# Kernel tuning notes

Hardware: AMD Instinct MI355X
Metric: run time of the kernel (lower is better)

The kernel has to match this reference:

```python
import jax, jax.numpy as jnp
import numpy as np

_FP8_MAX = 448.0  # finfo(float8_e4m3fn).max


def _quantize_fp8(w):
    """Per-tensor FP8 quantization: returns fp8-snapped weight (as f32) and scale."""
    scale = jnp.maximum(jnp.max(jnp.abs(w)).astype(jnp.float32) / _FP8_MAX, 1e-12)
    w_q = (w / scale).astype(jnp.float8_e4m3fn).astype(jnp.float32)
    return w_q, scale


def setup_inputs() -> dict:
    key = jax.random.key(0)
    k_x, k_g, k_u, k_d = jax.random.split(key, 4)
    B, S, H, I = 4, 2048, 4096, 11008
    x = jax.random.normal(k_x, (B, S, H), dtype=jnp.float32)
    gate = jax.random.normal(k_g, (I, H), dtype=jnp.float32) * 0.05
    up = jax.random.normal(k_u, (I, H), dtype=jnp.float32) * 0.05
    down = jax.random.normal(k_d, (H, I), dtype=jnp.float32) * 0.05
    gate_w, gate_w_scale = _quantize_fp8(gate)
    up_w, up_w_scale = _quantize_fp8(up)
    down_w, down_w_scale = _quantize_fp8(down)
    one = jnp.float32(1.0)
    return {
        "x": x,
        "gate_w": gate_w, "up_w": up_w, "down_w": down_w,
        "gate_w_scale": gate_w_scale, "up_w_scale": up_w_scale, "down_w_scale": down_w_scale,
        "gate_in_scale": one, "up_in_scale": one, "down_in_scale": one,
    }


def _fake_quant_fp8_linear(x, w_q, in_scale, w_scale):
    # Fake-quantize activations to FP8 (per-tensor scale), dequantize weight, GEMM.
    x_q = jnp.clip(x / in_scale, -_FP8_MAX, _FP8_MAX)
    x_dq = x_q.astype(jnp.float8_e4m3fn).astype(jnp.float32) * in_scale
    w_dq = w_q * w_scale  # w_q values are already on the FP8 grid
    return jnp.einsum('bsh,ih->bsi', x_dq, w_dq)


def reference(x, gate_w, up_w, down_w, gate_w_scale, up_w_scale, down_w_scale,
              gate_in_scale, up_in_scale, down_in_scale):
    gate_out = _fake_quant_fp8_linear(x, gate_w, gate_in_scale, gate_w_scale)
    up_out = _fake_quant_fp8_linear(x, up_w, up_in_scale, up_w_scale)
    hidden = jax.nn.silu(gate_out) * up_out  # SwiGLU
    return _fake_quant_fp8_linear(hidden, down_w, down_in_scale, down_w_scale)
```

## Files before the change

### kernel.cpp

```cpp
#include <hip/hip_runtime.h>
#include <stdint.h>


typedef float f32x4 __attribute__((ext_vector_type(4)));
typedef int   i32x4 __attribute__((ext_vector_type(4)));
typedef int   i32x8 __attribute__((ext_vector_type(8)));
typedef unsigned int u32;

#define AS1 __attribute__((address_space(1)))
#define AS3 __attribute__((address_space(3)))

#define TM 128
#define TN 128
#define BM1 256
#define BN1 128
#define BKB 128

#define SCALE1 0x7F7F7F7F

__device__ __forceinline__ void gld_lds16(const uint8_t* g, uint8_t* l) {
  __builtin_amdgcn_global_load_lds((const AS1 u32*)g, (AS3 u32*)l, 16, 0, 0);
}

__device__ __forceinline__ uint8_t f32_to_fp8(float v) {
  v = fminf(fmaxf(v, -448.f), 448.f);
  int r = __builtin_amdgcn_cvt_pk_fp8_f32(v, v, 0, false);
  return (uint8_t)(r & 0xff);
}

__device__ __forceinline__ i32x8 read_frag32(const uint8_t* s, int row, int ko, int swz) {
  const uint8_t* p = s + row * BKB;
  i32x4 lo = *(const i32x4*)(p + ((ko) ^ swz));
  i32x4 hi = *(const i32x4*)(p + ((ko + 16) ^ swz));
  return __builtin_shufflevector(lo, hi, 0, 1, 2, 3, 4, 5, 6, 7);
}

__global__ __launch_bounds__(256) void quant_fp8_k(const float* __restrict__ in,
                                                   uint8_t* __restrict__ out,
                                                   const float* __restrict__ scale_ptr,
                                                   long n8) {
  long i = (long)blockIdx.x * 256 + threadIdx.x;
  if (i >= n8) return;
  float inv = scale_ptr ? (1.0f / scale_ptr[0]) : 1.0f;
  const float4* p = (const float4*)(in + i * 8);
  float4 a = p[0], b = p[1];
  float v0 = fminf(fmaxf(a.x * inv, -448.f), 448.f);
  float v1 = fminf(fmaxf(a.y * inv, -448.f), 448.f);
  float v2 = fminf(fmaxf(a.z * inv, -448.f), 448.f);
  float v3 = fminf(fmaxf(a.w * inv, -448.f), 448.f);
  float v4 = fminf(fmaxf(b.x * inv, -448.f), 448.f);
  float v5 = fminf(fmaxf(b.y * inv, -448.f), 448.f);
  float v6 = fminf(fmaxf(b.z * inv, -448.f), 448.f);
  float v7 = fminf(fmaxf(b.w * inv, -448.f), 448.f);
  int lo = __builtin_amdgcn_cvt_pk_fp8_f32(v0, v1, 0, false);
  lo = __builtin_amdgcn_cvt_pk_fp8_f32(v2, v3, lo, true);
  int hi = __builtin_amdgcn_cvt_pk_fp8_f32(v4, v5, 0, false);
  hi = __builtin_amdgcn_cvt_pk_fp8_f32(v6, v7, hi, true);
  ((int2*)out)[i] = make_int2(lo, hi);
}

__global__ __launch_bounds__(512, 2) void gemm1_swiglu(
    const uint8_t* __restrict__ Xq,
    const uint8_t* __restrict__ Gq,
    const uint8_t* __restrict__ Uq,
    uint8_t* __restrict__ Hq,
    const float* __restrict__ gws, const float* __restrict__ uws,
    const float* __restrict__ gis, const float* __restrict__ uis,
    const float* __restrict__ dis,
    int M, int H, int I) {
  __shared__ uint8_t sX[2][BM1 * BKB];
  __shared__ uint8_t sG[2][BN1 * BKB];
  __shared__ uint8_t sU[2][BN1 * BKB];

  const int tid = threadIdx.x;
  const int wave = tid >> 6, lane = tid & 63;
  const int wr = wave >> 1, wc = wave & 1;
  const int lrow = lane & 15;
  const int lkg = lane >> 4;
  const int swz = (lrow & 7) << 4;
  const int ko = lkg * 32;

  const int GX = 43, GY = 8;
  const int g = blockIdx.x & 7;
  const int w = blockIdx.x >> 3;
  const int ggx = g & 1, ggy = g >> 1;
  const int xb = ggx * GX + w / GY;
  const int yb = ggy * GY + (w % GY);
  const int bM = yb * BM1, bN = xb * BN1;

  f32x4 accG[4][4] = {};
  f32x4 accU[4][4] = {};

  const uint8_t* gx = Xq + (size_t)bM * H;
  const uint8_t* gg = Gq + (size_t)bN * H;
  const uint8_t* gu = Uq + (size_t)bN * H;

  auto stage_x = [&](int buf, int it, int k0) {
    int c = it * 512 + tid;
    int r = c >> 3;
    int col = ((c & 7) ^ (r & 7)) * 16;
    gld_lds16(gx + (size_t)r * H + k0 + col, &sX[buf][(it * 8 + wave) * 1024]);
  };
  auto stage_g = [&](int buf, int it, int k0) {
    int c = it * 512 + tid;
    int r = c >> 3;
    int col = ((c & 7) ^ (r & 7)) * 16;
    gld_lds16(gg + (size_t)r * H + k0 + col, &sG[buf][(it * 8 + wave) * 1024]);
  };
  auto stage_u = [&](int buf, int it, int k0) {
    int c = it * 512 + tid;
    int r = c >> 3;
    int col = ((c & 7) ^ (r & 7)) * 16;
    gld_lds16(gu + (size_t)r * H + k0 + col, &sU[buf][(it * 8 + wave) * 1024]);
  };

  const int NK = H / BKB;

  stage_x(0, 0, 0); stage_x(0, 1, 0); stage_x(0, 2, 0); stage_x(0, 3, 0);
  stage_g(0, 0, 0); stage_g(0, 1, 0); stage_u(0, 0, 0); stage_u(0, 1, 0);

  for (int t = 0; t < NK; ++t) {
    const int cur = t & 1, nxt = cur ^ 1;
    const int k1 = (t + 1) * BKB;
    const bool pre = (t + 1 < NK);

    if (pre) { stage_x(nxt, 0, k1); stage_g(nxt, 0, k1); }
    if (pre) asm volatile("s_waitcnt vmcnt(2)" ::: "memory");
    else     asm volatile("s_waitcnt vmcnt(0)" ::: "memory");
    __builtin_amdgcn_s_barrier();

    i32x8 af[4];
#pragma unroll
    for (int i = 0; i < 4; ++i)
      af[i] = read_frag32(&sX[cur][0], wr * 64 + i * 16 + lrow, ko, swz);

#pragma unroll
    for (int j = 0; j < 4; ++j) {
      i32x8 gf = read_frag32(&sG[cur][0], wc * 64 + j * 16 + lrow, ko, swz);
      i32x8 uf = read_frag32(&sU[cur][0], wc * 64 + j * 16 + lrow, ko, swz);
      if (pre) {
        if (j == 1)      { stage_x(nxt, 1, k1); stage_g(nxt, 1, k1); }
        else if (j == 2) { stage_x(nxt, 2, k1); stage_u(nxt, 0, k1); }
        else if (j == 3) { stage_x(nxt, 3, k1); stage_u(nxt, 1, k1); }
      }
      __builtin_amdgcn_s_setprio(1);
#pragma unroll
      for (int i = 0; i < 4; ++i) {
        accG[i][j] = __builtin_amdgcn_mfma_scale_f32_16x16x128_f8f6f4(
            af[i], gf, accG[i][j], 0, 0, 0, SCALE1, 0, SCALE1);
        accU[i][j] = __builtin_amdgcn_mfma_scale_f32_16x16x128_f8f6f4(
            af[i], uf, accU[i][j], 0, 0, 0, SCALE1, 0, SCALE1);
      }
      __builtin_amdgcn_s_setprio(0);
    }
    asm volatile("s_waitcnt lgkmcnt(0)" ::: "memory");
    __builtin_amdgcn_s_barrier();
  }

  const float sg = gws[0] * gis[0];
  const float su = uws[0] * uis[0];
  const float invd = 1.0f / dis[0];

  uint8_t* sH = &sX[0][0];

#pragma unroll
  for (int i = 0; i < 4; ++i)
#pragma unroll
    for (int j = 0; j < 4; ++j)
#pragma unroll
      for (int tt = 0; tt < 4; ++tt) {
        float g2 = accG[i][j][tt] * sg;
        float u = accU[i][j][tt] * su;
        float h = (g2 / (1.0f + expf(-g2))) * u * invd;
        int row = wr * 64 + i * 16 + lkg * 4 + tt;
        int col = wc * 64 + j * 16 + lrow;
        sH[row * BN1 + col] = f32_to_fp8(h);
      }
  __syncthreads();
#pragma unroll
  for (int it = 0; it < 4; ++it) {
    int o = (it * 512 + tid) * 16;
    int row = o >> 7, col = o & 127;
    *(int4*)(Hq + (size_t)(bM + row) * I + bN + col) = *(const int4*)(sH + o);
  }
}

__global__ __launch_bounds__(256, 2) void gemm2_down(
    const uint8_t* __restrict__ Hq,
    const uint8_t* __restrict__ Dq,
    float* __restrict__ Out,
    const float* __restrict__ dws, const float* __restrict__ dis,
    int M, int I, int Hd) {
  __shared__ uint8_t sA[TM * BKB];
  __shared__ uint8_t sB[2 * TN * BKB];

  const int tid = threadIdx.x;
  const int wave = tid >> 6, lane = tid & 63;
  const int wr = wave >> 1, wc = wave & 1;
  const int lrow = lane & 15;
  const int lkg = lane >> 4;
  const int swz = (lrow & 7) << 4;
  const int ko = lkg * 32;

  const int g = blockIdx.x >> 8, w = blockIdx.x & 255;
  const int xb = w >> 4;
  const int yb = (g << 4) + (w & 15);
  const int bM = yb * TM, bN = xb * 256;

  f32x4 acc[4][8] = {};

  const uint8_t* ga = Hq + (size_t)bM * I;
  const uint8_t* gb = Dq + (size_t)bN * I;

  for (int k0 = 0; k0 < I; k0 += BKB) {
    if (k0) __syncthreads();
#pragma unroll
    for (int it = 0; it < 4; ++it) {
      int c = it * 256 + tid;
      int r = c >> 3;
      int col = ((c & 7) ^ (r & 7)) * 16;
      gld_lds16(ga + (size_t)r * I + k0 + col, sA + (it * 4 + wave) * 1024);
    }
#pragma unroll
    for (int it = 0; it < 8; ++it) {
      int c = it * 256 + tid;
      int r = c >> 3;
      int col = ((c & 7) ^ (r & 7)) * 16;
      gld_lds16(gb + (size_t)r * I + k0 + col, sB + (it * 4 + wave) * 1024);
    }
    asm volatile("s_waitcnt vmcnt(0)" ::: "memory");
    __syncthreads();

    i32x8 af[4];
#pragma unroll
    for (int i = 0; i < 4; ++i)
      af[i] = read_frag32(sA, wr * 64 + i * 16 + lrow, ko, swz);
#pragma unroll
    for (int j = 0; j < 8; ++j) {
      i32x8 bf = read_frag32(sB, wc * 128 + j * 16 + lrow, ko, swz);
#pragma unroll
      for (int i = 0; i < 4; ++i)
        acc[i][j] = __builtin_amdgcn_mfma_scale_f32_16x16x128_f8f6f4(
            af[i], bf, acc[i][j], 0, 0, 0, SCALE1, 0, SCALE1);
    }
  }

  const float ds = dws[0] * dis[0];
#pragma unroll
  for (int i = 0; i < 4; ++i)
#pragma unroll
    for (int j = 0; j < 8; ++j) {
      int row = bM + wr * 64 + i * 16 + lkg * 4;
      int col = bN + wc * 128 + j * 16 + lrow;
#pragma unroll
      for (int t = 0; t < 4; ++t)
        Out[(size_t)(row + t) * Hd + col] = acc[i][j][t] * ds;
    }
}

extern "C" void kernel_launch(void* const* d_in, const int* in_sizes, int n_in,
                              void* d_out, int out_size, void* d_ws, size_t ws_size,
                              hipStream_t stream) {
  const float* x   = (const float*)d_in[0];
  const float* gw  = (const float*)d_in[1];
  const float* uw  = (const float*)d_in[2];
  const float* dw  = (const float*)d_in[3];
  const float* gws = (const float*)d_in[4];
  const float* uws = (const float*)d_in[5];
  const float* dws = (const float*)d_in[6];
  const float* gis = (const float*)d_in[7];
  const float* uis = (const float*)d_in[8];
  const float* dis = (const float*)d_in[9];

  const int Hd = 4096;
  const int M  = in_sizes[0] / Hd;
  const int I  = in_sizes[1] / Hd;

  const size_t szX = (size_t)M * Hd;
  const size_t szW = (size_t)I * Hd;
  const size_t szH = (size_t)M * I;

  uint8_t* xq = (uint8_t*)d_ws;
  uint8_t* gq = xq + szX;
  uint8_t* uq = gq + szW;
  uint8_t* hq = uq + szW;
  uint8_t* dq = gq;

  if (ws_size < szX + 2 * szW + szH) return;

  float* out = (float*)d_out;

  {
    long n8 = (long)(szX / 8);
    quant_fp8_k<<<dim3((n8 + 255) / 256), dim3(256), 0, stream>>>(x, xq, gis, n8);
  }
  {
    long n8 = (long)(szW / 8);
    quant_fp8_k<<<dim3((n8 + 255) / 256), dim3(256), 0, stream>>>(gw, gq, nullptr, n8);
    quant_fp8_k<<<dim3((n8 + 255) / 256), dim3(256), 0, stream>>>(uw, uq, nullptr, n8);
  }

  gemm1_swiglu<<<dim3((I / BN1) * (M / BM1)), dim3(512), 0, stream>>>(
      xq, gq, uq, hq, gws, uws, gis, uis, dis, M, Hd, I);

  {
    long n8 = (long)(szW / 8);
    quant_fp8_k<<<dim3((n8 + 255) / 256), dim3(256), 0, stream>>>(dw, dq, nullptr, n8);
  }
  gemm2_down<<<dim3((Hd / 256) * (M / TM)), dim3(256), 0, stream>>>(
      hq, dq, out, dws, dis, M, I, Hd);
}
```

Before: 1.467 ms.

## Double-buffer down GEMM B tiles and add per-subtile barriers in gate/up GEMM

```diff
diff --git a/kernel.cpp b/kernel.cpp
--- a/kernel.cpp
+++ b/kernel.cpp
@@ -81,8 +81,8 @@
   const int ko = lkg * 32;
 
   const int GX = 43, GY = 8;
-  const int g = blockIdx.x & 7;
-  const int w = blockIdx.x >> 3;
+  const int per = GX * GY;
+  const int g = blockIdx.x / per, w = blockIdx.x % per;
   const int ggx = g & 1, ggy = g >> 1;
   const int xb = ggx * GX + w / GY;
   const int yb = ggy * GY + (w % GY);
@@ -124,25 +124,45 @@
     const int k1 = (t + 1) * BKB;
     const bool pre = (t + 1 < NK);
 
-    if (pre) { stage_x(nxt, 0, k1); stage_g(nxt, 0, k1); }
-    if (pre) asm volatile("s_waitcnt vmcnt(2)" ::: "memory");
-    else     asm volatile("s_waitcnt vmcnt(0)" ::: "memory");
+    if (pre) {
+      stage_x(nxt, 0, k1); stage_g(nxt, 0, k1);
+      asm volatile("s_waitcnt vmcnt(2)" ::: "memory");
+    } else {
+      asm volatile("s_waitcnt vmcnt(0)" ::: "memory");
+    }
     __builtin_amdgcn_s_barrier();
 
     i32x8 af[4];
 #pragma unroll
     for (int i = 0; i < 4; ++i)
       af[i] = read_frag32(&sX[cur][0], wr * 64 + i * 16 + lrow, ko, swz);
-
-#pragma unroll
-    for (int j = 0; j < 4; ++j) {
+    {
+      i32x8 gf = read_frag32(&sG[cur][0], wc * 64 + 0 * 16 + lrow, ko, swz);
+      i32x8 uf = read_frag32(&sU[cur][0], wc * 64 + 0 * 16 + lrow, ko, swz);
+      asm volatile("s_waitcnt lgkmcnt(0)" ::: "memory");
+      __builtin_amdgcn_s_setprio(1);
+#pragma unroll
+      for (int i = 0; i < 4; ++i) {
+        accG[i][0] = __builtin_amdgcn_mfma_scale_f32_16x16x128_f8f6f4(
+            af[i], gf, accG[i][0], 0, 0, 0, SCALE1, 0, SCALE1);
+        accU[i][0] = __builtin_amdgcn_mfma_scale_f32_16x16x128_f8f6f4(
+            af[i], uf, accU[i][0], 0, 0, 0, SCALE1, 0, SCALE1);
+      }
+      __builtin_amdgcn_s_setprio(0);
+    }
+    __builtin_amdgcn_s_barrier();
+
+#pragma unroll
+    for (int j = 1; j < 4; ++j) {
       i32x8 gf = read_frag32(&sG[cur][0], wc * 64 + j * 16 + lrow, ko, swz);
       i32x8 uf = read_frag32(&sU[cur][0], wc * 64 + j * 16 + lrow, ko, swz);
       if (pre) {
         if (j == 1)      { stage_x(nxt, 1, k1); stage_g(nxt, 1, k1); }
         else if (j == 2) { stage_x(nxt, 2, k1); stage_u(nxt, 0, k1); }
-        else if (j == 3) { stage_x(nxt, 3, k1); stage_u(nxt, 1, k1); }
+        else             { stage_x(nxt, 3, k1); stage_u(nxt, 1, k1); }
       }
+      __builtin_amdgcn_s_barrier();
+      asm volatile("s_waitcnt lgkmcnt(0)" ::: "memory");
       __builtin_amdgcn_s_setprio(1);
 #pragma unroll
       for (int i = 0; i < 4; ++i) {
@@ -152,9 +172,8 @@
             af[i], uf, accU[i][j], 0, 0, 0, SCALE1, 0, SCALE1);
       }
       __builtin_amdgcn_s_setprio(0);
-    }
-    asm volatile("s_waitcnt lgkmcnt(0)" ::: "memory");
-    __builtin_amdgcn_s_barrier();
+      __builtin_amdgcn_s_barrier();
+    }
   }
 
   const float sg = gws[0] * gis[0];
@@ -192,7 +211,7 @@
     const float* __restrict__ dws, const float* __restrict__ dis,
     int M, int I, int Hd) {
   __shared__ uint8_t sA[TM * BKB];
-  __shared__ uint8_t sB[2 * TN * BKB];
+  __shared__ uint8_t sB[2][2 * TN * BKB];
 
   const int tid = threadIdx.x;
   const int wave = tid >> 6, lane = tid & 63;
@@ -212,8 +231,7 @@
   const uint8_t* ga = Hq + (size_t)bM * I;
   const uint8_t* gb = Dq + (size_t)bN * I;
 
-  for (int k0 = 0; k0 < I; k0 += BKB) {
-    if (k0) __syncthreads();
+  auto stageA = [&](int k0) {
 #pragma unroll
     for (int it = 0; it < 4; ++it) {
       int c = it * 256 + tid;
@@ -221,15 +239,30 @@
       int col = ((c & 7) ^ (r & 7)) * 16;
       gld_lds16(ga + (size_t)r * I + k0 + col, sA + (it * 4 + wave) * 1024);
     }
+  };
+  auto stageB = [&](int buf, int k0) {
 #pragma unroll
     for (int it = 0; it < 8; ++it) {
       int c = it * 256 + tid;
       int r = c >> 3;
       int col = ((c & 7) ^ (r & 7)) * 16;
-      gld_lds16(gb + (size_t)r * I + k0 + col, sB + (it * 4 + wave) * 1024);
-    }
-    asm volatile("s_waitcnt vmcnt(0)" ::: "memory");
-    __syncthreads();
+      gld_lds16(gb + (size_t)r * I + k0 + col, &sB[buf][(it * 4 + wave) * 1024]);
+    }
+  };
+
+  const int NK = I / BKB;
+  stageB(0, 0);
+
+  for (int t = 0; t < NK; ++t) {
+    const int cur = t & 1, nxt = cur ^ 1;
+    stageA(t * BKB);
+    if (t + 1 < NK) {
+      stageB(nxt, (t + 1) * BKB);
+      asm volatile("s_waitcnt vmcnt(8)" ::: "memory");
+    } else {
+      asm volatile("s_waitcnt vmcnt(0)" ::: "memory");
+    }
+    __builtin_amdgcn_s_barrier();
 
     i32x8 af[4];
 #pragma unroll
@@ -237,12 +270,14 @@
       af[i] = read_frag32(sA, wr * 64 + i * 16 + lrow, ko, swz);
 #pragma unroll
     for (int j = 0; j < 8; ++j) {
-      i32x8 bf = read_frag32(sB, wc * 128 + j * 16 + lrow, ko, swz);
+      i32x8 bf = read_frag32(&sB[cur][0], wc * 128 + j * 16 + lrow, ko, swz);
 #pragma unroll
       for (int i = 0; i < 4; ++i)
         acc[i][j] = __builtin_amdgcn_mfma_scale_f32_16x16x128_f8f6f4(
             af[i], bf, acc[i][j], 0, 0, 0, SCALE1, 0, SCALE1);
     }
+    asm volatile("s_waitcnt lgkmcnt(0)" ::: "memory");
+    __builtin_amdgcn_s_barrier();
   }
 
   const float ds = dws[0] * dis[0];
```

After: 1.508 ms. 2.8% more time.
